# Kernel optimization log

Measured on AMD Instinct MI355X. Metric: run time of the kernel, lower is better.

The kernel has to match this reference:

```python
import jax, jax.numpy as jnp
import numpy as np

N_NODES = 100000
HIDDEN = 128


def _gcn_conv(x, edge_index, W, b, n_nodes):
    # PyG GCNConv with default symmetric normalization and self-loops.
    src, dst = edge_index[0], edge_index[1]
    loop = jnp.arange(n_nodes, dtype=src.dtype)
    src = jnp.concatenate([src, loop])
    dst = jnp.concatenate([dst, loop])
    # degree over destination nodes (edge weight = 1), self-loops included
    deg = jax.ops.segment_sum(jnp.ones_like(dst, dtype=x.dtype), dst,
                              num_segments=n_nodes)
    dinv = jax.lax.rsqrt(deg)  # deg >= 1 because of self-loops
    norm = dinv[src] * dinv[dst]  # [E+N]
    h = x @ W  # [N, 4H] linear transform first (d_in -> 4H)
    msg = norm[:, None] * h[src]  # [E+N, 4H]
    out = jax.ops.segment_sum(msg, dst, num_segments=n_nodes)
    return out + b


def setup_inputs() -> dict:
    key = jax.random.key(0)
    k1, k2, k3, k4, k5, k6 = jax.random.split(key, 6)
    n, h = N_NODES, HIDDEN
    x = jax.random.normal(k1, (n, h), dtype=jnp.float32)
    h_cur = jax.random.normal(k2, (n, h), dtype=jnp.float32)
    c_cur = jax.random.normal(k3, (n, h), dtype=jnp.float32)
    edge_index = jax.random.randint(k4, (2, 3200000), 0, n, dtype=jnp.int64)
    W = jax.random.normal(k5, (h, 4 * h), dtype=jnp.float32) / np.sqrt(h)
    b = jax.random.normal(k6, (4 * h,), dtype=jnp.float32) * 0.01
    return {"x": x, "edge_index": edge_index, "h_cur": h_cur,
            "c_cur": c_cur, "W": W, "b": b}


def reference(x, edge_index, h_cur, c_cur, W, b):
    combined = x + h_cur  # fused input + hidden add
    conv = _gcn_conv(combined, edge_index, W, b, x.shape[0])  # [N, 4H]
    cc_f = conv[:, :HIDDEN]  # first gate chunk (module returns cc_f only)
    return cc_f
```

## Files before the change

### kernel.cpp

```cpp
#include <hip/hip_runtime.h>
#include <hip/hip_bf16.h>

#define HID 128
#define BSH 6
#define MAXBUCK 2048
#define CAP 2816

__device__ __forceinline__ float b2f(unsigned short u) {
    union { unsigned i; float f; } v; v.i = ((unsigned)u) << 16; return v.f;
}
__device__ __forceinline__ unsigned short f2b(float f) {
    unsigned u = __float_as_uint(f);
    return (unsigned short)((u + 0x7fffu + ((u >> 16) & 1u)) >> 16);
}

__global__ void zero_kernel(unsigned* __restrict__ p, int n) {
    int i = blockIdx.x * blockDim.x + threadIdx.x;
    if (i < n) p[i] = 0u;
}

__global__ __launch_bounds__(256) void bincount_kernel(const int* __restrict__ ei,
                                                       unsigned* __restrict__ bcount,
                                                       int E, int n, int nbuck) {
    __shared__ unsigned hist[MAXBUCK];
    for (int i = threadIdx.x; i < nbuck; i += 256) hist[i] = 0u;
    __syncthreads();
    int i = blockIdx.x * 256 + threadIdx.x, stride = gridDim.x * 256;
    for (; i < E; i += stride) {
        int dst = ei[(size_t)E + i];
        if ((unsigned)dst < (unsigned)n) atomicAdd(&hist[dst >> BSH], 1u);
    }
    __syncthreads();
    for (int b = threadIdx.x; b < nbuck; b += 256) {
        unsigned c = hist[b];
        if (c) atomicAdd(&bcount[b], c);
    }
}

__global__ __launch_bounds__(1024) void bscan_kernel(const unsigned* __restrict__ bcount,
                                                     unsigned* __restrict__ boff,
                                                     unsigned* __restrict__ bwoff,
                                                     int nbuck) {
    __shared__ unsigned sums[1024];
    int t = threadIdx.x;
    int chunk = (nbuck + 1023) >> 10;
    int beg = min(t * chunk, nbuck), end = min(beg + chunk, nbuck);
    unsigned local = 0;
    for (int i = beg; i < end; ++i) local += bcount[i];
    sums[t] = local;
    __syncthreads();
    for (int d = 1; d < 1024; d <<= 1) {
        unsigned v = (t >= d) ? sums[t - d] : 0u;
        __syncthreads();
        sums[t] += v;
        __syncthreads();
    }
    unsigned run = (t > 0) ? sums[t - 1] : 0u;
    for (int i = beg; i < end; ++i) { boff[i] = run; bwoff[i] = run; run += bcount[i]; }
    if (t == 1023) boff[nbuck] = sums[1023];
}

__global__ __launch_bounds__(256) void phase3_kernel(const int* __restrict__ ei,
                                                     unsigned* __restrict__ bwoff,
                                                     unsigned* __restrict__ binned,
                                                     const float* __restrict__ x,
                                                     const float* __restrict__ hc,
                                                     const float* __restrict__ W,
                                                     unsigned short* __restrict__ hp,
                                                     int E, int n, int nbuck, int nsb) {
    __shared__ union {
        struct { unsigned hist[MAXBUCK]; unsigned base[MAXBUCK]; } bs;
        float A[64 * 132];
    } sm;

    if (blockIdx.x < nsb) {
        int chunk = (E + nsb - 1) / nsb;
        int beg = blockIdx.x * chunk, end = min(E, beg + chunk);
        for (int i = threadIdx.x; i < nbuck; i += 256) sm.bs.hist[i] = 0u;
        __syncthreads();
        for (int i = beg + threadIdx.x; i < end; i += 256) {
            int dst = ei[(size_t)E + i];
            if ((unsigned)dst < (unsigned)n) atomicAdd(&sm.bs.hist[dst >> BSH], 1u);
        }
        __syncthreads();
        for (int b = threadIdx.x; b < nbuck; b += 256) {
            unsigned c = sm.bs.hist[b];
            sm.bs.base[b] = c ? atomicAdd(&bwoff[b], c) : 0u;
            sm.bs.hist[b] = 0u;
        }
        __syncthreads();
        for (int i = beg + threadIdx.x; i < end; i += 256) {
            int s = ei[i];
            int dst = ei[(size_t)E + i];
            if ((unsigned)dst >= (unsigned)n) continue;
            unsigned ss = (unsigned)min(max(s, 0), n - 1);
            int b = dst >> BSH;
            unsigned r = atomicAdd(&sm.bs.hist[b], 1u);
            binned[sm.bs.base[b] + r] = ss | ((unsigned)(dst & ((1 << BSH) - 1)) << 20);
        }
    } else {
        int tid = threadIdx.x;
        int r0 = (blockIdx.x - nsb) * 64;

        for (int i = tid; i < 2048; i += 256) {
            int row = i >> 5;
            int c4 = (i & 31) * 4;
            int grow = r0 + row;
            float4 v;
            if (grow < n) {
                float4 a = *(const float4*)(x + (size_t)grow * HID + c4);
                float4 bb = *(const float4*)(hc + (size_t)grow * HID + c4);
                v = make_float4(a.x + bb.x, a.y + bb.y, a.z + bb.z, a.w + bb.w);
            } else {
                v = make_float4(0.f, 0.f, 0.f, 0.f);
            }
            *(float4*)(&sm.A[row * 132 + c4]) = v;
        }
        __syncthreads();

        int cg = tid & 31;
        int c4 = cg * 4;
        int rg = tid >> 5;
        float acc[8][4];
#pragma unroll
        for (int r = 0; r < 8; ++r) {
            acc[r][0] = 0.f; acc[r][1] = 0.f; acc[r][2] = 0.f; acc[r][3] = 0.f;
        }

#pragma unroll 4
        for (int k = 0; k < 128; ++k) {
            float4 w = *(const float4*)(W + (size_t)k * 512 + c4);
#pragma unroll
            for (int r = 0; r < 8; ++r) {
                float a = sm.A[(rg * 8 + r) * 132 + k];
                acc[r][0] += a * w.x;
                acc[r][1] += a * w.y;
                acc[r][2] += a * w.z;
                acc[r][3] += a * w.w;
            }
        }

#pragma unroll
        for (int r = 0; r < 8; ++r) {
            int grow = r0 + rg * 8 + r;
            if (grow < n) {
                unsigned long long pack =
                    (unsigned long long)f2b(acc[r][0]) |
                    ((unsigned long long)f2b(acc[r][1]) << 16) |
                    ((unsigned long long)f2b(acc[r][2]) << 32) |
                    ((unsigned long long)f2b(acc[r][3]) << 48);
                *(unsigned long long*)(hp + (size_t)grow * HID + c4) = pack;
            }
        }
    }
}

__global__ __launch_bounds__(256) void csrlite_kernel(const unsigned* __restrict__ binned,
                                                      const unsigned* __restrict__ boff,
                                                      unsigned* __restrict__ off,
                                                      float* __restrict__ dinv, int n) {
    __shared__ unsigned hist[64];
    int b = blockIdx.x;
    int t = threadIdx.x;
    if (t < 64) hist[t] = 0u;
    __syncthreads();
    unsigned s0 = boff[b], s1 = boff[b + 1];
    for (unsigned j = s0 + t; j < s1; j += 256) atomicAdd(&hist[binned[j] >> 20], 1u);
    __syncthreads();
    if (t < 64) {
        unsigned cnt = hist[t];
        unsigned x = cnt;
        for (int d = 1; d < 64; d <<= 1) {
            unsigned v = __shfl_up(x, d, 64);
            if (t >= d) x += v;
        }
        unsigned excl = x - cnt;
        int node = (b << BSH) + t;
        if (node < n) {
            off[node] = s0 + excl;
            dinv[node] = rsqrtf((float)(cnt + 1u));
        }
    }
}

__global__ __launch_bounds__(256) void agg_merged_kernel(const unsigned* __restrict__ binned,
                                                         const unsigned* __restrict__ boff,
                                                         const unsigned* __restrict__ off,
                                                         const float* __restrict__ dinv,
                                                         const unsigned short* __restrict__ hp,
                                                         const float* __restrict__ bias,
                                                         float* __restrict__ out, int n) {
    __shared__ unsigned srcs_lds[CAP];
    __shared__ unsigned nodeoff[65];
    __shared__ unsigned cursor[64];
    __shared__ float sdinv[64];
    int b = blockIdx.x;
    int tid = threadIdx.x;
    unsigned s0 = boff[b], s1 = boff[b + 1];
    unsigned cnt = s1 - s0;
    int node0 = b << BSH;

    if (tid < 64) {
        int node = node0 + tid;
        unsigned o = (node < n) ? off[node] : s1;
        nodeoff[tid] = o - s0;
        cursor[tid] = o - s0;
        sdinv[tid] = (node < n) ? dinv[node] : 0.f;
    }
    if (tid == 64) nodeoff[64] = cnt;
    __syncthreads();

    if (cnt <= CAP) {
        for (unsigned j = s0 + tid; j < s1; j += 256) {
            unsigned p = binned[j];
            unsigned slot = atomicAdd(&cursor[p >> 20], 1u);
            srcs_lds[slot] = p & 0xFFFFFu;
        }
        __syncthreads();

        int w = tid >> 6, lane = tid & 63;
        int c = lane * 2;
        for (int nl = w * 16; nl < w * 16 + 16; ++nl) {
            int node = node0 + nl;
            if (node >= n) break;
            unsigned beg = nodeoff[nl], end2 = nodeoff[nl + 1];
            float ax = 0.f, ay = 0.f;
            unsigned i = beg;
            for (; i + 8 <= end2; i += 8) {
                unsigned s[8]; float wd[8]; ushort2 v[8];
#pragma unroll
                for (int j = 0; j < 8; ++j) s[j] = srcs_lds[i + j];
#pragma unroll
                for (int j = 0; j < 8; ++j) wd[j] = dinv[s[j]];
#pragma unroll
                for (int j = 0; j < 8; ++j) v[j] = *(const ushort2*)(hp + ((size_t)s[j] << 7) + c);
#pragma unroll
                for (int j = 0; j < 8; ++j) { ax += wd[j] * b2f(v[j].x); ay += wd[j] * b2f(v[j].y); }
            }
            if (i < end2) {
                unsigned last = end2 - 1;
                unsigned s[8]; float wd[8]; ushort2 v[8];
#pragma unroll
                for (int j = 0; j < 8; ++j) {
                    unsigned jj = i + j;
                    s[j] = srcs_lds[jj < end2 ? jj : last];
                    wd[j] = (jj < end2) ? 1.f : 0.f;
                }
#pragma unroll
                for (int j = 0; j < 8; ++j) wd[j] *= dinv[s[j]];
#pragma unroll
                for (int j = 0; j < 8; ++j) v[j] = *(const ushort2*)(hp + ((size_t)s[j] << 7) + c);
#pragma unroll
                for (int j = 0; j < 8; ++j) { ax += wd[j] * b2f(v[j].x); ay += wd[j] * b2f(v[j].y); }
            }
            float dd = sdinv[nl];
            ushort2 hd = *(const ushort2*)(hp + ((size_t)node << 7) + c);
            ax += dd * b2f(hd.x);
            ay += dd * b2f(hd.y);
            float2 bb = *(const float2*)(bias + c);
            float2 res = make_float2(dd * ax + bb.x, dd * ay + bb.y);
            *(float2*)(out + ((size_t)node << 7) + c) = res;
        }
    } else {
        for (int idx = tid; idx < 64 * HID; idx += 256) {
            int ndl = idx >> 7, col = idx & (HID - 1);
            int node = node0 + ndl;
            if (node < n) {
                float dd = sdinv[ndl];
                out[((size_t)node << 7) + col] = dd * dd * b2f(hp[((size_t)node << 7) + col]) + bias[col];
            }
        }
        __syncthreads();
        if (tid < 64) {
            int c = tid * 2;
            for (unsigned j = s0; j < s1; ++j) {
                unsigned p = binned[j];
                unsigned dl = p >> 20, s = p & 0xFFFFFu;
                float wsc = dinv[s] * sdinv[dl];
                ushort2 v = *(const ushort2*)(hp + ((size_t)s << 7) + c);
                float2* o = (float2*)(out + ((size_t)(node0 + dl) << 7) + c);
                float2 cur = *o;
                cur.x += wsc * b2f(v.x);
                cur.y += wsc * b2f(v.y);
                *o = cur;
            }
        }
    }
}

extern "C" void kernel_launch(void* const* d_in, const int* in_sizes, int n_in,
                              void* d_out, int out_size, void* d_ws, size_t ws_size,
                              hipStream_t stream) {
    const float* x = (const float*)d_in[0];
    const int* ei = (const int*)d_in[1];
    const float* hc = (const float*)d_in[2];
    const float* W = (const float*)d_in[4];
    const float* b = (const float*)d_in[5];
    float* out = (float*)d_out;

    int n = in_sizes[0] / HID;
    int E = in_sizes[1] / 2;
    int nbuck = (n + 63) >> BSH;
    int nsb = 256;

    char* ws = (char*)d_ws;
    unsigned* bcount = (unsigned*)(ws);
    unsigned* boff   = (unsigned*)(ws + 8192);
    unsigned* bwoff  = (unsigned*)(ws + 16384);
    unsigned* off    = (unsigned*)(ws + 24576);
    float*    dinv   = (float*)   (ws + 424576);
    unsigned* binned = (unsigned*)(ws + 824576);
    unsigned short* hp = (unsigned short*)(ws + 13624576);

    zero_kernel<<<(nbuck + 255) / 256, 256, 0, stream>>>(bcount, nbuck);
    bincount_kernel<<<512, 256, 0, stream>>>(ei, bcount, E, n, nbuck);
    bscan_kernel<<<1, 1024, 0, stream>>>(bcount, boff, bwoff, nbuck);

    int gemm_blocks = (n + 63) / 64;
    phase3_kernel<<<nsb + gemm_blocks, 256, 0, stream>>>(ei, bwoff, binned, x, hc, W, hp,
                                                         E, n, nbuck, nsb);
    csrlite_kernel<<<nbuck, 256, 0, stream>>>(binned, boff, off, dinv, n);
    agg_merged_kernel<<<nbuck, 256, 0, stream>>>(binned, boff, off, dinv, hp, b, out, n);
}
```

Baseline: 241.9 us.

## Replace atomic bucket reservation with per-block histogram and 2D scan

```diff
diff --git a/kernel.cpp b/kernel.cpp
--- a/kernel.cpp
+++ b/kernel.cpp
@@ -4,6 +4,7 @@
 #define HID 128
 #define BSH 6
 #define MAXBUCK 2048
+#define NSB 512
 #define CAP 2816
 
 __device__ __forceinline__ float b2f(unsigned short u) {
@@ -14,32 +15,53 @@
     return (unsigned short)((u + 0x7fffu + ((u >> 16) & 1u)) >> 16);
 }
 
-__global__ void zero_kernel(unsigned* __restrict__ p, int n) {
-    int i = blockIdx.x * blockDim.x + threadIdx.x;
-    if (i < n) p[i] = 0u;
-}
-
-__global__ __launch_bounds__(256) void bincount_kernel(const int* __restrict__ ei,
-                                                       unsigned* __restrict__ bcount,
-                                                       int E, int n, int nbuck) {
-    __shared__ unsigned hist[MAXBUCK];
-    for (int i = threadIdx.x; i < nbuck; i += 256) hist[i] = 0u;
-    __syncthreads();
-    int i = blockIdx.x * 256 + threadIdx.x, stride = gridDim.x * 256;
-    for (; i < E; i += stride) {
+__global__ __launch_bounds__(256) void histblk_kernel(const int* __restrict__ ei,
+                                                      unsigned* __restrict__ hist,
+                                                      int E, int n, int nbuck) {
+    __shared__ unsigned h[MAXBUCK];
+    for (int i = threadIdx.x; i < nbuck; i += 256) h[i] = 0u;
+    __syncthreads();
+    int blk = blockIdx.x;
+    int chunk = (E + NSB - 1) / NSB;
+    int beg = blk * chunk, end = min(E, beg + chunk);
+    for (int i = beg + threadIdx.x; i < end; i += 256) {
         int dst = ei[(size_t)E + i];
-        if ((unsigned)dst < (unsigned)n) atomicAdd(&hist[dst >> BSH], 1u);
-    }
-    __syncthreads();
-    for (int b = threadIdx.x; b < nbuck; b += 256) {
-        unsigned c = hist[b];
-        if (c) atomicAdd(&bcount[b], c);
-    }
+        if ((unsigned)dst < (unsigned)n) atomicAdd(&h[dst >> BSH], 1u);
+    }
+    __syncthreads();
+    for (int b = threadIdx.x; b < nbuck; b += 256)
+        hist[(size_t)blk * nbuck + b] = h[b];
+}
+
+__global__ __launch_bounds__(256) void scan2d_kernel(const unsigned* __restrict__ hist,
+                                                     unsigned* __restrict__ base_rel,
+                                                     unsigned* __restrict__ bcount,
+                                                     int nbuck) {
+    int b = blockIdx.x;
+    int t = threadIdx.x;
+    unsigned v0 = hist[(size_t)(2 * t) * nbuck + b];
+    unsigned v1 = hist[(size_t)(2 * t + 1) * nbuck + b];
+    unsigned pair = v0 + v1;
+    int lane = t & 63, w = t >> 6;
+    unsigned x = pair;
+    for (int d = 1; d < 64; d <<= 1) {
+        unsigned y = __shfl_up(x, d, 64);
+        if (lane >= d) x += y;
+    }
+    __shared__ unsigned wsum[4];
+    if (lane == 63) wsum[w] = x;
+    __syncthreads();
+    unsigned add = 0;
+    for (int ww = 0; ww < 4; ++ww) if (ww < w) add += wsum[ww];
+    unsigned incl = x + add;
+    unsigned excl = incl - pair;
+    base_rel[(size_t)(2 * t) * nbuck + b] = excl;
+    base_rel[(size_t)(2 * t + 1) * nbuck + b] = excl + v0;
+    if (t == 255) bcount[b] = incl;
 }
 
 __global__ __launch_bounds__(1024) void bscan_kernel(const unsigned* __restrict__ bcount,
                                                      unsigned* __restrict__ boff,
-                                                     unsigned* __restrict__ bwoff,
                                                      int nbuck) {
     __shared__ unsigned sums[1024];
     int t = threadIdx.x;
@@ -56,53 +78,44 @@
         __syncthreads();
     }
     unsigned run = (t > 0) ? sums[t - 1] : 0u;
-    for (int i = beg; i < end; ++i) { boff[i] = run; bwoff[i] = run; run += bcount[i]; }
+    for (int i = beg; i < end; ++i) { boff[i] = run; run += bcount[i]; }
     if (t == 1023) boff[nbuck] = sums[1023];
 }
 
 __global__ __launch_bounds__(256) void phase3_kernel(const int* __restrict__ ei,
-                                                     unsigned* __restrict__ bwoff,
+                                                     const unsigned* __restrict__ boff,
+                                                     const unsigned* __restrict__ base_rel,
                                                      unsigned* __restrict__ binned,
                                                      const float* __restrict__ x,
                                                      const float* __restrict__ hc,
                                                      const float* __restrict__ W,
                                                      unsigned short* __restrict__ hp,
-                                                     int E, int n, int nbuck, int nsb) {
+                                                     int E, int n, int nbuck) {
     __shared__ union {
-        struct { unsigned hist[MAXBUCK]; unsigned base[MAXBUCK]; } bs;
-        float A[64 * 132];
+        unsigned cursor[MAXBUCK];
+        float A[32 * 132];
     } sm;
 
-    if (blockIdx.x < nsb) {
-        int chunk = (E + nsb - 1) / nsb;
-        int beg = blockIdx.x * chunk, end = min(E, beg + chunk);
-        for (int i = threadIdx.x; i < nbuck; i += 256) sm.bs.hist[i] = 0u;
-        __syncthreads();
-        for (int i = beg + threadIdx.x; i < end; i += 256) {
-            int dst = ei[(size_t)E + i];
-            if ((unsigned)dst < (unsigned)n) atomicAdd(&sm.bs.hist[dst >> BSH], 1u);
-        }
-        __syncthreads();
-        for (int b = threadIdx.x; b < nbuck; b += 256) {
-            unsigned c = sm.bs.hist[b];
-            sm.bs.base[b] = c ? atomicAdd(&bwoff[b], c) : 0u;
-            sm.bs.hist[b] = 0u;
-        }
-        __syncthreads();
+    if (blockIdx.x < NSB) {
+        int blk = blockIdx.x;
+        for (int b = threadIdx.x; b < nbuck; b += 256)
+            sm.cursor[b] = boff[b] + base_rel[(size_t)blk * nbuck + b];
+        __syncthreads();
+        int chunk = (E + NSB - 1) / NSB;
+        int beg = blk * chunk, end = min(E, beg + chunk);
         for (int i = beg + threadIdx.x; i < end; i += 256) {
             int s = ei[i];
             int dst = ei[(size_t)E + i];
             if ((unsigned)dst >= (unsigned)n) continue;
             unsigned ss = (unsigned)min(max(s, 0), n - 1);
-            int b = dst >> BSH;
-            unsigned r = atomicAdd(&sm.bs.hist[b], 1u);
-            binned[sm.bs.base[b] + r] = ss | ((unsigned)(dst & ((1 << BSH) - 1)) << 20);
+            unsigned slot = atomicAdd(&sm.cursor[dst >> BSH], 1u);
+            binned[slot] = ss | ((unsigned)(dst & ((1 << BSH) - 1)) << 20);
         }
     } else {
         int tid = threadIdx.x;
-        int r0 = (blockIdx.x - nsb) * 64;
-
-        for (int i = tid; i < 2048; i += 256) {
+        int r0 = (blockIdx.x - NSB) * 32;
+
+        for (int i = tid; i < 1024; i += 256) {
             int row = i >> 5;
             int c4 = (i & 31) * 4;
             int grow = r0 + row;
@@ -121,9 +134,9 @@
         int cg = tid & 31;
         int c4 = cg * 4;
         int rg = tid >> 5;
-        float acc[8][4];
-#pragma unroll
-        for (int r = 0; r < 8; ++r) {
+        float acc[4][4];
+#pragma unroll
+        for (int r = 0; r < 4; ++r) {
             acc[r][0] = 0.f; acc[r][1] = 0.f; acc[r][2] = 0.f; acc[r][3] = 0.f;
         }
 
@@ -131,8 +144,8 @@
         for (int k = 0; k < 128; ++k) {
             float4 w = *(const float4*)(W + (size_t)k * 512 + c4);
 #pragma unroll
-            for (int r = 0; r < 8; ++r) {
-                float a = sm.A[(rg * 8 + r) * 132 + k];
+            for (int r = 0; r < 4; ++r) {
+                float a = sm.A[(rg * 4 + r) * 132 + k];
                 acc[r][0] += a * w.x;
                 acc[r][1] += a * w.y;
                 acc[r][2] += a * w.z;
@@ -141,8 +154,8 @@
         }
 
 #pragma unroll
-        for (int r = 0; r < 8; ++r) {
-            int grow = r0 + rg * 8 + r;
+        for (int r = 0; r < 4; ++r) {
+            int grow = r0 + rg * 4 + r;
             if (grow < n) {
                 unsigned long long pack =
                     (unsigned long long)f2b(acc[r][0]) |
@@ -301,24 +314,25 @@
     int n = in_sizes[0] / HID;
     int E = in_sizes[1] / 2;
     int nbuck = (n + 63) >> BSH;
-    int nsb = 256;
 
     char* ws = (char*)d_ws;
     unsigned* bcount = (unsigned*)(ws);
     unsigned* boff   = (unsigned*)(ws + 8192);
-    unsigned* bwoff  = (unsigned*)(ws + 16384);
     unsigned* off    = (unsigned*)(ws + 24576);
     float*    dinv   = (float*)   (ws + 424576);
     unsigned* binned = (unsigned*)(ws + 824576);
     unsigned short* hp = (unsigned short*)(ws + 13624576);
 
-    zero_kernel<<<(nbuck + 255) / 256, 256, 0, stream>>>(bcount, nbuck);
-    bincount_kernel<<<512, 256, 0, stream>>>(ei, bcount, E, n, nbuck);
-    bscan_kernel<<<1, 1024, 0, stream>>>(bcount, boff, bwoff, nbuck);
-
-    int gemm_blocks = (n + 63) / 64;
-    phase3_kernel<<<nsb + gemm_blocks, 256, 0, stream>>>(ei, bwoff, binned, x, hc, W, hp,
-                                                         E, n, nbuck, nsb);
+    unsigned* hist     = (unsigned*)d_out;
+    unsigned* base_rel = hist + (size_t)NSB * nbuck;
+
+    histblk_kernel<<<NSB, 256, 0, stream>>>(ei, hist, E, n, nbuck);
+    scan2d_kernel<<<nbuck, 256, 0, stream>>>(hist, base_rel, bcount, nbuck);
+    bscan_kernel<<<1, 1024, 0, stream>>>(bcount, boff, nbuck);
+
+    int gemm_blocks = (n + 31) / 32;
+    phase3_kernel<<<NSB + gemm_blocks, 256, 0, stream>>>(ei, boff, base_rel, binned,
+                                                         x, hc, W, hp, E, n, nbuck);
     csrlite_kernel<<<nbuck, 256, 0, stream>>>(binned, boff, off, dinv, n);
     agg_merged_kernel<<<nbuck, 256, 0, stream>>>(binned, boff, off, dinv, hp, b, out, n);
 }
```

Result: no change. 246.6 us (+1.9%).
